# Kernel tuning notes

Hardware: AMD Instinct MI355X
Metric: run time of the kernel (lower is better)

## Reference

```python
import jax, jax.numpy as jnp
import numpy as np

# --- static configuration (mirrors PMETorchPME(alpha=1.0, mesh=1.0), interpolation_nodes=6) ---
ALPHA = 1.0            # Gaussian smearing sigma of CoulombPotential
MESH_SPACING = 1.0
BOX_L = 120.0
NS = (120, 120, 120)   # ceil(BOX_L / MESH_SPACING) per axis; static for jit
ORDER = 6              # interpolation nodes (6-point stencil per axis)
N_ATOMS = 100000
PI = np.pi


def _interp_weights(x):
    # x: (N,3) offsets in [-0.5, 0.5) relative to the midpoint of the 6-point stencil.
    # Lagrange interpolation on nodes t_j = j - 2.5, j = 0..5 (even-order, midpoint-centered).
    t = np.arange(ORDER) - (ORDER - 1) / 2.0                 # (6,) node positions
    diff = x[..., None] - jnp.asarray(t, x.dtype)            # (N,3,6)
    ws = []
    for j in range(ORDER):
        idx = [k for k in range(ORDER) if k != j]
        denom = float(np.prod([t[j] - t[k] for k in idx]))
        ws.append(jnp.prod(diff[..., idx], axis=-1) / denom)
    return jnp.stack(ws, axis=-1)                            # (N,3,6)


def _stencil(coords, box):
    # Map positions to mesh units, build per-particle 6x6x6 stencil weights + flat mesh indices.
    frac = coords @ jnp.linalg.inv(box)                      # fractional coordinates
    pos = frac * jnp.asarray(NS, coords.dtype)               # (N,3) in mesh units
    i0 = jnp.floor(pos)
    x = pos - (i0 + 0.5)                                     # offset from stencil midpoint
    w = _interp_weights(x)                                   # (N,3,6)
    offs = jnp.arange(ORDER, dtype=jnp.int32) - (ORDER // 2 - 1)   # [-2..3]
    ns_i = jnp.asarray(NS, jnp.int32)
    g = (i0.astype(jnp.int32)[..., None] + offs) % ns_i[None, :, None]  # (N,3,6) periodic
    W = w[:, 0, :, None, None] * w[:, 1, None, :, None] * w[:, 2, None, None, :]   # (N,6,6,6)
    flat = (g[:, 0, :, None, None] * NS[1] + g[:, 1, None, :, None]) * NS[2] + g[:, 2, None, None, :]
    n = coords.shape[0]
    return W.reshape(n, -1), flat.reshape(n, -1)             # (N,216) each


def _kspace_kernel(box, dtype):
    # G(k) = 4*pi * exp(-sigma^2 k^2 / 2) / k^2, zero at k=0 (CoulombPotential.lr_from_k_sq)
    inv_cell = jnp.linalg.inv(box)
    m0 = jnp.fft.fftfreq(NS[0]) * NS[0]
    m1 = jnp.fft.fftfreq(NS[1]) * NS[1]
    m2 = jnp.fft.rfftfreq(NS[2]) * NS[2]
    m = jnp.stack(jnp.meshgrid(m0, m1, m2, indexing="ij"), axis=-1).astype(dtype)
    k = 2.0 * PI * jnp.einsum("xyzm,nm->xyzn", m, inv_cell)  # k = 2*pi * inv(cell) @ m
    k_sq = jnp.sum(k * k, axis=-1)
    safe = jnp.where(k_sq > 0, k_sq, 1.0)
    return jnp.where(k_sq > 0, 4.0 * PI * jnp.exp(-0.5 * ALPHA * ALPHA * k_sq) / safe, 0.0)


def setup_inputs() -> dict:
    key = jax.random.key(0)
    k1, k2 = jax.random.split(key)
    coords = jax.random.uniform(k1, (N_ATOMS, 3), dtype=jnp.float32) * BOX_L
    box = (BOX_L * jnp.eye(3, dtype=jnp.float32))
    charges = jax.random.normal(k2, (N_ATOMS, 1), dtype=jnp.float32)
    return {"coords": coords, "box": box, "charges": charges}


def reference(coords, box, charges):
    q = charges[:, 0]                                        # (N,)
    W, flat = _stencil(coords, box)                          # (N,216)
    ntot = NS[0] * NS[1] * NS[2]
    # charge spreading (scatter-add)
    mesh = jnp.zeros((ntot,), coords.dtype).at[flat.reshape(-1)].add((W * q[:, None]).reshape(-1))
    mesh = mesh.reshape(NS)
    # FFT convolution with the reciprocal-space Coulomb kernel
    G = _kspace_kernel(box, coords.dtype)
    pot_mesh = jnp.fft.irfftn(jnp.fft.rfftn(mesh, norm="backward") * G, s=NS, norm="forward")
    # gather back to particles
    pot = jnp.sum(pot_mesh.reshape(-1)[flat] * W, axis=-1)   # (N,)
    volume = jnp.abs(jnp.linalg.det(box))
    pot = pot / volume
    pot = pot - q * (np.sqrt(2.0 / PI) / ALPHA)              # remove self-contribution
    pot = pot - 2.0 * (PI * ALPHA * ALPHA) * jnp.sum(q) / volume  # charge-neutral background
    pot = pot / 2.0
    return jnp.sum(q * pot)                                  # energy = sum(charges * potentials)
```

## Files before the change

kernel.cpp:

```cpp
#include <hip/hip_runtime.h>
#include <math.h>

#define NMESH 120
#define NKZ 61
#define ALPHA_C 1.0

#define TILE 12
#define NTPD 10
#define NTILE 1000
#define FP 17
#define ZPAD 20
#define FPSTRIDE 5792
#define CAP 256

#define CHUNK 128
#define WXA_OFF 0
#define WYA_OFF (CHUNK*17)
#define WZA_OFF (2*CHUNK*17)
#define LYS_OFF (2*CHUNK*17 + CHUNK*20)
#define SMEMF   (LYS_OFF + CHUNK)

#define YCH 12
#define XCH 4
#define YROW 137

#define NSLOT 64
#define SLOTSTRIDE 8
#define W120C (-0.052359877559829887f)

typedef float v2f __attribute__((ext_vector_type(2)));

#define EK_OFF      0
#define Q_OFF       4096
#define Q2_OFF      8192
#define BUF_OFF     115264
#define C1_OFF      23283264
#define C2_OFF      115264
#define COUNTS_OFF  C1_OFF
#define SORTED_OFF  (C1_OFF + 4096)

__device__ inline void inv3(const float* b, float* ib) {
    float a00=b[0],a01=b[1],a02=b[2],a10=b[3],a11=b[4],a12=b[5],a20=b[6],a21=b[7],a22=b[8];
    float c00 =  a11*a22 - a12*a21;
    float c01 = -(a10*a22 - a12*a20);
    float c02 =  a10*a21 - a11*a20;
    float c10 = -(a01*a22 - a02*a21);
    float c11 =  a00*a22 - a02*a20;
    float c12 = -(a00*a21 - a01*a20);
    float c20 =  a01*a12 - a02*a11;
    float c21 = -(a00*a12 - a02*a10);
    float c22 =  a00*a11 - a01*a10;
    float det = a00*c00 + a01*c01 + a02*c02;
    float inv = 1.0f/det;
    ib[0]=c00*inv; ib[1]=c10*inv; ib[2]=c20*inv;
    ib[3]=c01*inv; ib[4]=c11*inv; ib[5]=c21*inv;
    ib[6]=c02*inv; ib[7]=c12*inv; ib[8]=c22*inv;
}

__device__ inline void atom_pos(const float* __restrict__ box, float c0, float c1, float c2,
                                float* p) {
    float ib[9]; inv3(box, ib);
    #pragma unroll
    for (int d=0; d<3; ++d)
        p[d] = (c0*ib[0+d] + c1*ib[3+d] + c2*ib[6+d]) * 120.0f;
}

__device__ inline int wrap120(int i) { return ((i % 120) + 120) % 120; }

__device__ inline void lag6(float x, float* w) {
    float df[6];
    #pragma unroll
    for (int k=0;k<6;++k) df[k] = x - ((float)k - 2.5f);
    w[0] = df[1]*df[2]*df[3]*df[4]*df[5] * (-1.0f/120.0f);
    w[1] = df[0]*df[2]*df[3]*df[4]*df[5] * ( 1.0f/24.0f);
    w[2] = df[0]*df[1]*df[3]*df[4]*df[5] * (-1.0f/12.0f);
    w[3] = df[0]*df[1]*df[2]*df[4]*df[5] * ( 1.0f/12.0f);
    w[4] = df[0]*df[1]*df[2]*df[3]*df[5] * (-1.0f/24.0f);
    w[5] = df[0]*df[1]*df[2]*df[3]*df[4] * ( 1.0f/120.0f);
}

__device__ inline int halo_pairs(int c, int* t, int* l) {
    int r = c % 12, ti = c / 12, n = 0;
    t[n] = ti;          l[n] = r + 2;  n++;
    if (r < 3)  { t[n] = (ti+9)%10; l[n] = r + 14; n++; }
    if (r >= 10){ t[n] = (ti+1)%10; l[n] = r - 10; n++; }
    return n;
}

__device__ inline void dft8(const float2* xin, float2* Y) {
    const float S = 0.70710678118654752f;
    float2 a=xin[0], b=xin[2], c=xin[4], d=xin[6];
    float s02r=a.x+c.x, s02i=a.y+c.y, d02r=a.x-c.x, d02i=a.y-c.y;
    float s13r=b.x+d.x, s13i=b.y+d.y, d13r=b.x-d.x, d13i=b.y-d.y;
    float2 E0 = make_float2(s02r+s13r, s02i+s13i);
    float2 E1 = make_float2(d02r+d13i, d02i-d13r);
    float2 E2 = make_float2(s02r-s13r, s02i-s13i);
    float2 E3 = make_float2(d02r-d13i, d02i+d13r);
    a=xin[1]; b=xin[3]; c=xin[5]; d=xin[7];
    s02r=a.x+c.x; s02i=a.y+c.y; d02r=a.x-c.x; d02i=a.y-c.y;
    s13r=b.x+d.x; s13i=b.y+d.y; d13r=b.x-d.x; d13i=b.y-d.y;
    float2 O0 = make_float2(s02r+s13r, s02i+s13i);
    float2 O1 = make_float2(d02r+d13i, d02i-d13r);
    float2 O2 = make_float2(s02r-s13r, s02i-s13i);
    float2 O3 = make_float2(d02r-d13i, d02i+d13r);
    float t1r = S*(O1.x + O1.y), t1i = S*(O1.y - O1.x);
    float t2r = O2.y,            t2i = -O2.x;
    float t3r = S*(O3.y - O3.x), t3i = -S*(O3.x + O3.y);
    Y[0] = make_float2(E0.x + O0.x, E0.y + O0.y);
    Y[4] = make_float2(E0.x - O0.x, E0.y - O0.y);
    Y[1] = make_float2(E1.x + t1r,  E1.y + t1i);
    Y[5] = make_float2(E1.x - t1r,  E1.y - t1i);
    Y[2] = make_float2(E2.x + t2r,  E2.y + t2i);
    Y[6] = make_float2(E2.x - t2r,  E2.y - t2i);
    Y[3] = make_float2(E3.x + t3r,  E3.y + t3i);
    Y[7] = make_float2(E3.x - t3r,  E3.y - t3i);
}

__global__ void scatter_q_kernel(const float* __restrict__ coords,
                                 const float* __restrict__ box,
                                 const float* __restrict__ charges,
                                 int* __restrict__ counts,
                                 float4* __restrict__ sorted,
                                 double* __restrict__ qslots,
                                 double* __restrict__ q2slots, int n) {
    int i = blockIdx.x*blockDim.x + threadIdx.x;
    float v = 0.f, v2 = 0.f;
    if (i < n) {
        float p[3]; atom_pos(box, coords[3*i], coords[3*i+1], coords[3*i+2], p);
        float q = charges[i];
        v = q; v2 = q*q;
        int t[3];
        #pragma unroll
        for (int d=0; d<3; ++d) t[d] = wrap120((int)floorf(p[d])) / TILE;
        int tile = (t[0]*NTPD + t[1])*NTPD + t[2];
        int idx = atomicAdd(&counts[tile], 1);
        if (idx < CAP) sorted[tile*CAP + idx] = make_float4(p[0], p[1], p[2], q);
    }
    #pragma unroll
    for (int o=32;o>0;o>>=1) { v += __shfl_down(v,o,64); v2 += __shfl_down(v2,o,64); }
    __shared__ float s1[4], s2[4];
    int lane = threadIdx.x & 63, w = threadIdx.x >> 6;
    if (lane==0) { s1[w]=v; s2[w]=v2; }
    __syncthreads();
    if (threadIdx.x==0) {
        for (int j=1;j<4;j++) { v += s1[j]; v2 += s2[j]; }
        int slot = (blockIdx.x & (NSLOT-1)) * SLOTSTRIDE;
        atomicAdd(&qslots[slot],  (double)v);
        atomicAdd(&q2slots[slot], (double)v2);
    }
}

__global__ void __launch_bounds__(256, 4)
spread_tile_kernel(const float4* __restrict__ sorted,
                   const int* __restrict__ counts,
                   float* __restrict__ buf) {
    int tile = blockIdx.x;
    int tx = tile / (NTPD*NTPD);
    int rem = tile - tx*NTPD*NTPD;
    int ty = rem / NTPD;
    int tz = rem - ty*NTPD;
    int bx = tx*TILE, by = ty*TILE, bz = tz*TILE;

    __shared__ float smem[SMEMF];
    int* lys = (int*)&smem[LYS_OFF];

    int tid  = threadIdx.x;
    int wv   = tid >> 6;
    int lane = tid & 63;
    int half = wv & 1;
    int blo  = (wv < 2) ? 0 : 9;
    int t3   = lane / 17; if (t3 > 2) t3 = 2;
    int A    = lane - 17*t3; if (A > 16) A = 16;
    bool owner = (lane < 51);
    int B0   = blo + 3*t3;
    bool c2ok = (B0 + 2 <= 16);

    v2f   acc2[3][8];
    float acc16[3];
    #pragma unroll
    for (int c=0;c<3;++c) {
        #pragma unroll
        for (int k=0;k<8;++k) acc2[c][k] = (v2f){0.f,0.f};
        acc16[c] = 0.f;
    }

    int cntT = min(counts[tile], CAP);
    const float4* src = sorted + (size_t)tile*CAP;

    for (int start = 0; start < cntT; start += CHUNK) {
        int jn = cntT - start; if (jn > CHUNK) jn = CHUNK;
        __syncthreads();
        if (tid < jn) {
            float4 s = src[start + tid];
            float fx = floorf(s.x), fy = floorf(s.y), fz = floorf(s.z);
            float wx[6]; lag6(s.x - (fx + 0.5f), wx);
            float wy[6]; lag6(s.y - (fy + 0.5f), wy);
            float wz[6]; lag6(s.z - (fz + 0.5f), wz);
            int lx = wrap120((int)fx) - bx;
            int ly = wrap120((int)fy) - by;
            int lz = wrap120((int)fz) - bz;
            #pragma unroll
            for (int k=0;k<17;++k) { smem[WXA_OFF + tid*17 + k] = 0.f;
                                     smem[WYA_OFF + tid*17 + k] = 0.f; }
            float4 z4 = make_float4(0.f,0.f,0.f,0.f);
            float4* pz = (float4*)&smem[WZA_OFF + tid*ZPAD];
            #pragma unroll
            for (int k=0;k<5;++k) pz[k] = z4;
            #pragma unroll
            for (int k=0;k<6;++k) {
                smem[WXA_OFF + tid*17 + lx + k] = wx[k];
                smem[WYA_OFF + tid*17 + ly + k] = wy[k];
                smem[WZA_OFF + tid*ZPAD + lz + k] = wz[k]*s.w;
            }
            lys[tid] = ly;
        }
        __syncthreads();
        int j0  = half * 64;
        int idx = j0 + lane;
        int lyv = lys[idx];
        bool g = (idx < jn) && (blo ? (lyv >= 4) : (lyv <= 8));
        unsigned long long m = __ballot(g);
        while (m) {
            int j = j0 + __builtin_ctzll(m); m &= m - 1ull;
            float wx_ = smem[WXA_OFF + j*17 + A];
            float wy0 = smem[WYA_OFF + j*17 + B0];
            float wy1 = smem[WYA_OFF + j*17 + B0 + 1];
            float wy2 = smem[WYA_OFF + j*17 + B0 + 2];
            float w2c[3];
            w2c[0] = wx_*wy0;
            w2c[1] = wx_*wy1;
            w2c[2] = c2ok ? wx_*wy2 : 0.f;
            const float4* zp = (const float4*)&smem[WZA_OFF + j*ZPAD];
            float4 z0 = zp[0], z1 = zp[1], z2 = zp[2], z3 = zp[3];
            float z16 = smem[WZA_OFF + j*ZPAD + 16];
            v2f zz[8];
            zz[0]=(v2f){z0.x,z0.y}; zz[1]=(v2f){z0.z,z0.w};
            zz[2]=(v2f){z1.x,z1.y}; zz[3]=(v2f){z1.z,z1.w};
            zz[4]=(v2f){z2.x,z2.y}; zz[5]=(v2f){z2.z,z2.w};
            zz[6]=(v2f){z3.x,z3.y}; zz[7]=(v2f){z3.z,z3.w};
            #pragma unroll
            for (int c=0;c<3;++c) {
                v2f wv2 = (v2f){w2c[c], w2c[c]};
                #pragma unroll
                for (int k=0;k<8;++k) acc2[c][k] += wv2 * zz[k];
                acc16[c] = fmaf(w2c[c], z16, acc16[c]);
            }
        }
    }
    __syncthreads();
    if ((half == 0) && owner) {
        #pragma unroll
        for (int c=0;c<3;++c) {
            int Bc = B0 + c;
            if (Bc <= 16) {
                float* dst = &smem[(A*17 + Bc)*ZPAD];
                *(float4*)&dst[0]  = make_float4(acc2[c][0].x, acc2[c][0].y, acc2[c][1].x, acc2[c][1].y);
                *(float4*)&dst[4]  = make_float4(acc2[c][2].x, acc2[c][2].y, acc2[c][3].x, acc2[c][3].y);
                *(float4*)&dst[8]  = make_float4(acc2[c][4].x, acc2[c][4].y, acc2[c][5].x, acc2[c][5].y);
                *(float4*)&dst[12] = make_float4(acc2[c][6].x, acc2[c][6].y, acc2[c][7].x, acc2[c][7].y);
                dst[16] = acc16[c];
            }
        }
    }
    __syncthreads();
    if ((half == 1) && owner) {
        #pragma unroll
        for (int c=0;c<3;++c) {
            int Bc = B0 + c;
            if (Bc <= 16) {
                float* dst = &smem[(A*17 + Bc)*ZPAD];
                float4 a0 = *(float4*)&dst[0],  a1 = *(float4*)&dst[4];
                float4 a2 = *(float4*)&dst[8],  a3 = *(float4*)&dst[12];
                float  a4 = dst[16];
                *(float4*)&dst[0]  = make_float4(a0.x+acc2[c][0].x, a0.y+acc2[c][0].y, a0.z+acc2[c][1].x, a0.w+acc2[c][1].y);
                *(float4*)&dst[4]  = make_float4(a1.x+acc2[c][2].x, a1.y+acc2[c][2].y, a1.z+acc2[c][3].x, a1.w+acc2[c][3].y);
                *(float4*)&dst[8]  = make_float4(a2.x+acc2[c][4].x, a2.y+acc2[c][4].y, a2.z+acc2[c][5].x, a2.w+acc2[c][5].y);
                *(float4*)&dst[12] = make_float4(a3.x+acc2[c][6].x, a3.y+acc2[c][6].y, a3.z+acc2[c][7].x, a3.w+acc2[c][7].y);
                dst[16] = a4 + acc16[c];
            }
        }
    }
    __syncthreads();
    float4* bp = (float4*)(buf + (size_t)tile * FPSTRIDE);
    const float4* sp = (const float4*)smem;
    for (int i = tid; i < FPSTRIDE/4; i += 256) bp[i] = sp[i];
}

#define DFT15_BODY(Yp, kfreq, RE, IM)                                        \
    float w1r = tw[kfreq].x, w1i = tw[kfreq].y;                              \
    float w2r = w1r*w1r - w1i*w1i, w2i = 2.f*w1r*w1i;                        \
    float w3r = w2r*w1r - w2i*w1i, w3i = w2r*w1i + w2i*w1r;                  \
    float ar=1.f, ai=0.f, br=w1r, bi=w1i, cr=w2r, ci=w2i;                    \
    float r0_=0.f,i0_=0.f,r1_=0.f,i1_=0.f,r2_=0.f,i2_=0.f;                   \
    _Pragma("unroll")                                                        \
    for (int s_=0;s_<5;++s_) {                                               \
        float2 ya = (Yp)[3*s_], yb = (Yp)[3*s_+1], yc = (Yp)[3*s_+2];        \
        r0_ = fmaf(ya.x, ar, fmaf(-ya.y, ai, r0_));                          \
        i0_ = fmaf(ya.x, ai, fmaf( ya.y, ar, i0_));                          \
        r1_ = fmaf(yb.x, br, fmaf(-yb.y, bi, r1_));                          \
        i1_ = fmaf(yb.x, bi, fmaf( yb.y, br, i1_));                          \
        r2_ = fmaf(yc.x, cr, fmaf(-yc.y, ci, r2_));                          \
        i2_ = fmaf(yc.x, ci, fmaf( yc.y, cr, i2_));                          \
        float n_;                                                            \
        n_ = ar*w3r - ai*w3i; ai = ar*w3i + ai*w3r; ar = n_;                 \
        n_ = br*w3r - bi*w3i; bi = br*w3i + bi*w3r; br = n_;                 \
        n_ = cr*w3r - ci*w3i; ci = cr*w3i + ci*w3r; cr = n_;                 \
    }                                                                        \
    float RE = (r0_+r1_)+r2_, IM = (i0_+i1_)+i2_;

#define TWIDDLE_INIT()                                                       \
    __shared__ float2 tw[120];                                               \
    for (int k_ = threadIdx.x; k_ < 120; k_ += blockDim.x) {                 \
        float s_, c_; __sincosf(W120C * (float)k_, &s_, &c_);                \
        tw[k_] = make_float2(c_, s_);                                        \
    }

__global__ void __launch_bounds__(256)
fft_z_kernel(const float* __restrict__ buf,
             float2* __restrict__ C1) {
    int x  = blockIdx.x / 10;
    int y0 = (blockIdx.x - x*10) * YCH;
    __shared__ float  lin[YCH][121];
    __shared__ float2 Ys[YCH][YROW];
    TWIDDLE_INIT()

    int txA[2], lxA[2];
    int nx = halo_pairs(x, txA, lxA);

    for (int i = threadIdx.x; i < YCH*120; i += 256) {
        int yl = i / 120, z = i - yl*120;
        int tyA[2], lyA[2]; int ny = halo_pairs(y0 + yl, tyA, lyA);
        int tzA[2], lzA[2]; int nz = halo_pairs(z, tzA, lzA);
        float s = 0.f;
        for (int ii=0; ii<nx; ++ii)
            for (int jj=0; jj<ny; ++jj)
                for (int kk=0; kk<nz; ++kk) {
                    int tile = (txA[ii]*NTPD + tyA[jj])*NTPD + tzA[kk];
                    int cell = (lxA[ii]*FP + lyA[jj])*ZPAD + lzA[kk];
                    s += buf[(size_t)tile*FPSTRIDE + cell];
                }
        lin[yl][z] = s;
    }
    __syncthreads();
    for (int t = threadIdx.x; t < YCH*15; t += 256) {
        int yl = t / 15, j = t - (t/15)*15;
        float2 xin[8], Yo[8];
        #pragma unroll
        for (int m=0;m<8;++m) xin[m] = make_float2(lin[yl][15*m+j], 0.f);
        dft8(xin, Yo);
        #pragma unroll
        for (int r=0;r<8;++r) Ys[yl][r*17+j] = Yo[r];
    }
    __syncthreads();
    for (int o = threadIdx.x; o < YCH*NKZ; o += 256) {
        int kz = o / YCH, yl = o - (o/YCH)*YCH;
        const float2* Yp = &Ys[yl][(kz&7)*17];
        DFT15_BODY(Yp, kz, re, im)
        C1[(x*NKZ + kz)*120 + y0 + yl] = make_float2(re, im);
    }
}

__global__ void __launch_bounds__(256)
fft_y_kernel(const float2* __restrict__ C1,
             float2* __restrict__ C2) {
    int xc = blockIdx.x / NKZ;
    int kz = blockIdx.x - xc*NKZ;
    int x0 = xc * XCH;
    __shared__ float2 lin[XCH][121];
    __shared__ float2 Ys[XCH][YROW];
    TWIDDLE_INIT()
    for (int i = threadIdx.x; i < XCH*120; i += 256) {
        int xo = i / 120, y = i - (i/120)*120;
        lin[xo][y] = C1[((x0+xo)*NKZ + kz)*120 + y];
    }
    __syncthreads();
    for (int t = threadIdx.x; t < XCH*15; t += 256) {
        int xo = t / 15, j = t - (t/15)*15;
        float2 xin[8], Yo[8];
        #pragma unroll
        for (int m=0;m<8;++m) xin[m] = lin[xo][15*m+j];
        dft8(xin, Yo);
        #pragma unroll
        for (int r=0;r<8;++r) Ys[xo][r*17+j] = Yo[r];
    }
    __syncthreads();
    for (int o = threadIdx.x; o < XCH*120; o += 256) {
        int ky = o >> 2, xo = o & 3;
        const float2* Yp = &Ys[xo][(ky&7)*17];
        DFT15_BODY(Yp, ky, re, im)
        C2[(kz*120 + ky)*120 + x0 + xo] = make_float2(re, im);
    }
}

__global__ void __launch_bounds__(256)
fft_x_energy_kernel(const float2* __restrict__ C2,
                    const float* __restrict__ box,
                    double* __restrict__ ekslots) {
    int kyc = blockIdx.x / NKZ;
    int kz  = blockIdx.x - kyc*NKZ;
    int ky0 = kyc * XCH;
    __shared__ float2 lin[XCH][121];
    __shared__ float2 Ys[XCH][YROW];
    TWIDDLE_INIT()
    const float2* src = C2 + (kz*120 + ky0)*120;
    for (int i = threadIdx.x; i < XCH*120; i += 256) {
        int kyo = i / 120, xx = i - (i/120)*120;
        lin[kyo][xx] = src[i];
    }
    __syncthreads();
    for (int t = threadIdx.x; t < XCH*15; t += 256) {
        int kyo = t / 15, j = t - (t/15)*15;
        float2 xin[8], Yo[8];
        #pragma unroll
        for (int m=0;m<8;++m) xin[m] = lin[kyo][15*m+j];
        dft8(xin, Yo);
        #pragma unroll
        for (int r=0;r<8;++r) Ys[kyo][r*17+j] = Yo[r];
    }
    __syncthreads();
    float ib[9]; inv3(box, ib);
    const float TWOPI = 6.283185307179586f;
    float wzf = (kz==0 || kz==60) ? 1.0f : 2.0f;
    float contrib = 0.f;
    for (int o = threadIdx.x; o < XCH*120; o += 256) {
        int kyo = o / 120, kx = o - (o/120)*120;
        int ky = ky0 + kyo;
        const float2* Yp = &Ys[kyo][(kx&7)*17];
        DFT15_BODY(Yp, kx, re, im)
        if (!(kx==0 && ky==0 && kz==0)) {
            float mx = (kx < 60) ? (float)kx : (float)(kx - 120);
            float my = (ky < 60) ? (float)ky : (float)(ky - 120);
            float mz = (float)kz;
            float k0 = TWOPI*(mx*ib[0] + my*ib[1] + mz*ib[2]);
            float k1 = TWOPI*(mx*ib[3] + my*ib[4] + mz*ib[5]);
            float k2 = TWOPI*(mx*ib[6] + my*ib[7] + mz*ib[8]);
            float ksq = k0*k0 + k1*k1 + k2*k2;
            float G = 12.566370614359172f * __expf(-0.5f*(float)(ALPHA_C*ALPHA_C)*ksq) / ksq;
            contrib += wzf * G * (re*re + im*im);
        }
    }
    #pragma unroll
    for (int o=32;o>0;o>>=1) contrib += __shfl_down(contrib,o,64);
    __shared__ float sm[4];
    int lane = threadIdx.x & 63, w = threadIdx.x >> 6;
    if (lane==0) sm[w] = contrib;
    __syncthreads();
    if (threadIdx.x==0)
        atomicAdd(&ekslots[(blockIdx.x & (NSLOT-1)) * SLOTSTRIDE],
                  (double)(sm[0]+sm[1]+sm[2]+sm[3]));
}

__global__ void finalize_kernel(const double* __restrict__ ekslots,
                                const double* __restrict__ qslots,
                                const double* __restrict__ q2slots,
                                const float* __restrict__ box,
                                float* __restrict__ out) {
    int lane = threadIdx.x;
    double ek  = ekslots[lane*SLOTSTRIDE];
    double sq  = qslots [lane*SLOTSTRIDE];
    double sq2 = q2slots[lane*SLOTSTRIDE];
    #pragma unroll
    for (int o=32;o>0;o>>=1) {
        ek  += __shfl_down(ek,  o, 64);
        sq  += __shfl_down(sq,  o, 64);
        sq2 += __shfl_down(sq2, o, 64);
    }
    if (lane == 0) {
        double a00=box[0],a01=box[1],a02=box[2],a10=box[3],a11=box[4],a12=box[5],a20=box[6],a21=box[7],a22=box[8];
        double det = a00*(a11*a22-a12*a21) - a01*(a10*a22-a12*a20) + a02*(a10*a21-a11*a20);
        double vol = fabs(det);
        double E = ek/(2.0*vol)
                 - 0.5*sqrt(2.0/M_PI)/ALPHA_C * sq2
                 - M_PI*ALPHA_C*ALPHA_C * sq*sq / vol;
        out[0] = (float)E;
    }
}

extern "C" void kernel_launch(void* const* d_in, const int* in_sizes, int n_in,
                              void* d_out, int out_size, void* d_ws, size_t ws_size,
                              hipStream_t stream) {
    const float* coords  = (const float*)d_in[0];
    const float* box     = (const float*)d_in[1];
    const float* charges = (const float*)d_in[2];
    int n = in_sizes[0] / 3;

    char* ws = (char*)d_ws;
    double* ekslots = (double*)(ws + EK_OFF);
    double* qslots  = (double*)(ws + Q_OFF);
    double* q2slots = (double*)(ws + Q2_OFF);
    float*  buf     = (float*) (ws + BUF_OFF);
    float2* C1      = (float2*)(ws + C1_OFF);
    float2* C2      = (float2*)(ws + C2_OFF);
    int* counts     = (int*)(ws + COUNTS_OFF);
    float4* sorted  = (float4*)(ws + SORTED_OFF);

    int gA = (n + 255)/256;
    hipMemsetAsync(ws + EK_OFF, 0, 3*4096, stream);
    hipMemsetAsync(ws + COUNTS_OFF, 0, NTILE*sizeof(int), stream);
    scatter_q_kernel<<<gA, 256, 0, stream>>>(coords, box, charges, counts, sorted, qslots, q2slots, n);
    spread_tile_kernel<<<NTILE, 256, 0, stream>>>(sorted, counts, buf);
    fft_z_kernel<<<120*10, 256, 0, stream>>>(buf, C1);
    fft_y_kernel<<<30*NKZ, 256, 0, stream>>>(C1, C2);
    fft_x_energy_kernel<<<NKZ*30, 256, 0, stream>>>(C2, box, ekslots);
    finalize_kernel<<<1, 64, 0, stream>>>(ekslots, qslots, q2slots, box, (float*)d_out);
}
```

Measured before the change: 150.1 us.

## Interleave particle split across wave halves, pad weight rows, merge memsets

The spread kernel's two wave halves now split particles by parity across both 64-particle groups instead of taking a contiguous half each. This balances work when a chunk is only partly filled. The x/y weight rows are padded to the 20-float stride so they can be zeroed with float4 stores. The counts buffer moves next to the slot accumulators so a single memset clears both. In exchange the kernel runs two ballot loops and uses somewhat more shared memory, and reads of lys entries beyond jn rely on the idx<jn guard.

```diff
diff --git a/kernel.cpp b/kernel.cpp
--- a/kernel.cpp
+++ b/kernel.cpp
@@ -15,9 +15,9 @@
 
 #define CHUNK 128
 #define WXA_OFF 0
-#define WYA_OFF (CHUNK*17)
-#define WZA_OFF (2*CHUNK*17)
-#define LYS_OFF (2*CHUNK*17 + CHUNK*20)
+#define WYA_OFF (CHUNK*ZPAD)
+#define WZA_OFF (2*CHUNK*ZPAD)
+#define LYS_OFF (3*CHUNK*ZPAD)
 #define SMEMF   (LYS_OFF + CHUNK)
 
 #define YCH 12
@@ -33,10 +33,10 @@
 #define EK_OFF      0
 #define Q_OFF       4096
 #define Q2_OFF      8192
+#define COUNTS_OFF  12288
 #define BUF_OFF     115264
 #define C1_OFF      23283264
 #define C2_OFF      115264
-#define COUNTS_OFF  C1_OFF
 #define SORTED_OFF  (C1_OFF + 4096)
 
 __device__ inline void inv3(const float* b, float* ib) {
@@ -199,33 +199,34 @@
             int lx = wrap120((int)fx) - bx;
             int ly = wrap120((int)fy) - by;
             int lz = wrap120((int)fz) - bz;
-            #pragma unroll
-            for (int k=0;k<17;++k) { smem[WXA_OFF + tid*17 + k] = 0.f;
-                                     smem[WYA_OFF + tid*17 + k] = 0.f; }
             float4 z4 = make_float4(0.f,0.f,0.f,0.f);
+            float4* px = (float4*)&smem[WXA_OFF + tid*ZPAD];
+            float4* py = (float4*)&smem[WYA_OFF + tid*ZPAD];
             float4* pz = (float4*)&smem[WZA_OFF + tid*ZPAD];
             #pragma unroll
-            for (int k=0;k<5;++k) pz[k] = z4;
+            for (int k=0;k<5;++k) { px[k]=z4; py[k]=z4; pz[k]=z4; }
             #pragma unroll
             for (int k=0;k<6;++k) {
-                smem[WXA_OFF + tid*17 + lx + k] = wx[k];
-                smem[WYA_OFF + tid*17 + ly + k] = wy[k];
+                smem[WXA_OFF + tid*ZPAD + lx + k] = wx[k];
+                smem[WYA_OFF + tid*ZPAD + ly + k] = wy[k];
                 smem[WZA_OFF + tid*ZPAD + lz + k] = wz[k]*s.w;
             }
             lys[tid] = ly;
         }
         __syncthreads();
-        int j0  = half * 64;
-        int idx = j0 + lane;
-        int lyv = lys[idx];
-        bool g = (idx < jn) && (blo ? (lyv >= 4) : (lyv <= 8));
-        unsigned long long m = __ballot(g);
-        while (m) {
-            int j = j0 + __builtin_ctzll(m); m &= m - 1ull;
-            float wx_ = smem[WXA_OFF + j*17 + A];
-            float wy0 = smem[WYA_OFF + j*17 + B0];
-            float wy1 = smem[WYA_OFF + j*17 + B0 + 1];
-            float wy2 = smem[WYA_OFF + j*17 + B0 + 2];
+        int idxA = lane, idxB = 64 + lane;
+        int lyA = lys[idxA], lyB = lys[idxB];
+        bool rA = blo ? (lyA >= 4) : (lyA <= 8);
+        bool rB = blo ? (lyB >= 4) : (lyB <= 8);
+        bool gA = (idxA < jn) && rA && ((idxA & 1) == half);
+        bool gB = (idxB < jn) && rB && ((idxB & 1) == half);
+        unsigned long long mA = __ballot(gA);
+        unsigned long long mB = __ballot(gB);
+        auto body = [&](int j) {
+            float wx_ = smem[WXA_OFF + j*ZPAD + A];
+            float wy0 = smem[WYA_OFF + j*ZPAD + B0];
+            float wy1 = smem[WYA_OFF + j*ZPAD + B0 + 1];
+            float wy2 = smem[WYA_OFF + j*ZPAD + B0 + 2];
             float w2c[3];
             w2c[0] = wx_*wy0;
             w2c[1] = wx_*wy1;
@@ -245,7 +246,9 @@
                 for (int k=0;k<8;++k) acc2[c][k] += wv2 * zz[k];
                 acc16[c] = fmaf(w2c[c], z16, acc16[c]);
             }
-        }
+        };
+        while (mA) { int j = __builtin_ctzll(mA); mA &= mA - 1ull; body(j); }
+        while (mB) { int j = 64 + __builtin_ctzll(mB); mB &= mB - 1ull; body(j); }
     }
     __syncthreads();
     if ((half == 0) && owner) {
@@ -495,8 +498,7 @@
     float4* sorted  = (float4*)(ws + SORTED_OFF);
 
     int gA = (n + 255)/256;
-    hipMemsetAsync(ws + EK_OFF, 0, 3*4096, stream);
-    hipMemsetAsync(ws + COUNTS_OFF, 0, NTILE*sizeof(int), stream);
+    hipMemsetAsync(ws, 0, 16384, stream);
     scatter_q_kernel<<<gA, 256, 0, stream>>>(coords, box, charges, counts, sorted, qslots, q2slots, n);
     spread_tile_kernel<<<NTILE, 256, 0, stream>>>(sorted, counts, buf);
     fft_z_kernel<<<120*10, 256, 0, stream>>>(buf, C1);
```

New measurement: 146.7 us (median of 2 runs). 1.02x faster.
